# Performance work log

Hardware: AMD Instinct MI355X
Metric: run time of the kernel (lower is better)

The kernel has to match this reference:

```python
import jax, jax.numpy as jnp
import numpy as np

N = 100000
E = 1600000
E_OUT = 400000
IN_DIM = 16
HID = 64
OUT_DIM = 2
L = 6
BN_EPS = 1e-5


def setup_inputs() -> dict:
    key = jax.random.key(0)
    ks = jax.random.split(key, 12)
    x = jax.random.normal(ks[0], (N, IN_DIM), dtype=jnp.float32)
    edge_index = jax.random.randint(ks[1], (2, E), 0, N, dtype=jnp.int64)
    edge_index_out = jax.random.randint(ks[2], (2, E_OUT), 0, N, dtype=jnp.int64)
    s_emb = 1.0 / np.sqrt(IN_DIM)
    s_hid = 1.0 / np.sqrt(HID)
    W_emb = jax.random.uniform(ks[3], (IN_DIM, HID), jnp.float32, -s_emb, s_emb)
    b_emb = jax.random.uniform(ks[4], (HID,), jnp.float32, -s_emb, s_emb)
    conv_W = jax.random.uniform(ks[5], (L, HID, HID), jnp.float32, -s_hid, s_hid)
    conv_b = jnp.zeros((L, HID), jnp.float32)
    bn_gamma = jnp.ones((L, HID), jnp.float32)
    bn_beta = jnp.zeros((L, HID), jnp.float32)
    s_fc = 1.0 / np.sqrt(2 * HID)
    fc_W = jax.random.uniform(ks[6], (2 * HID, OUT_DIM), jnp.float32, -s_fc, s_fc)
    fc_b = jax.random.uniform(ks[7], (OUT_DIM,), jnp.float32, -s_fc, s_fc)
    return dict(x=x, edge_index=edge_index, edge_index_out=edge_index_out,
                W_emb=W_emb, b_emb=b_emb, conv_W=conv_W, conv_b=conv_b,
                bn_gamma=bn_gamma, bn_beta=bn_beta, fc_W=fc_W, fc_b=fc_b)


def gcn_conv(h, W, b, src, dst, norm):
    # PyG GCNConv: h' = scatter_add(norm * (hW)[src] -> dst) + b
    hw = h @ W                                   # [N, HID]
    msgs = hw[src] * norm[:, None]               # [E+N, HID] gather
    agg = jax.ops.segment_sum(msgs, dst, num_segments=N)
    return agg + b


def batchnorm_train(h, gamma, beta):
    mean = jnp.mean(h, axis=0)
    var = jnp.mean(jnp.square(h - mean), axis=0)  # biased var (BN training)
    return (h - mean) * jax.lax.rsqrt(var + BN_EPS) * gamma + beta


def reference(x, edge_index, edge_index_out, W_emb, b_emb, conv_W, conv_b,
              bn_gamma, bn_beta, fc_W, fc_b):
    # add self-loops + symmetric normalization (computed once, shared by layers)
    loop = jnp.arange(N, dtype=edge_index.dtype)
    src = jnp.concatenate([edge_index[0], loop])
    dst = jnp.concatenate([edge_index[1], loop])
    deg = jax.ops.segment_sum(jnp.ones_like(dst, dtype=jnp.float32), dst, num_segments=N)
    dinv = jnp.where(deg > 0, jax.lax.rsqrt(jnp.maximum(deg, 1.0)), 0.0)
    norm = dinv[src] * dinv[dst]

    x_embed = x @ W_emb + b_emb                  # node embedding [N, HID]
    for i in range(L):
        h = gcn_conv(x_embed, conv_W[i], conv_b[i], src, dst, norm)
        h = jax.nn.relu(batchnorm_train(h, bn_gamma[i], bn_beta[i]))
        x_embed = x_embed + h                    # residual

    e_src, e_dst = edge_index_out[0], edge_index_out[1]
    edge_repr = jnp.concatenate([x_embed[e_src], x_embed[e_dst]], axis=-1)  # [E_out, 2*HID]
    return edge_repr @ fc_W + fc_b
```

## Files before the change

kernel.cpp:

```cpp
#include <hip/hip_runtime.h>

#define NN 100000
#define NE 1600000
#define NEO 400000
#define HID 64
#define NL 6
#define BN_EPS 1e-5f

#define SPMM_BLOCKS 6250
#define GRP_ROWS 12500

#define B1CAP 210000
#define BIN_CHUNK 1024
#define BIN_J (BIN_CHUNK / 256)
#define BIN_BLOCKS ((NE + BIN_CHUNK - 1) / BIN_CHUNK)
#define SB_PER_G 32
#define SB_ROWS 391
#define SBCAP 7600
#define BIN2_CHUNK 2048
#define BIN2_BPG 103

#define OFF_ECOL 0
#define OFF_XE   NE
#define OFF_AGG  (OFF_XE + NN * 32)
#define OFF_HWB  (OFF_AGG + NN * 32)

#define OD_DINV   0
#define OD_ROWPTR 100352
#define OD_SS     300960
#define OD_SUMS   301088
#define OD_GCUR   309280
#define OD_SCNT   309312
#define OD_SBASE  309568

typedef __attribute__((ext_vector_type(8))) short bf16x8;
typedef __attribute__((ext_vector_type(4))) float f32x4;

static __device__ __forceinline__ unsigned short f2bf(float f) {
    unsigned u = __float_as_uint(f);
    unsigned r = (u + 0x7FFF + ((u >> 16) & 1)) >> 16;
    return (unsigned short)r;
}
static __device__ __forceinline__ float bflo(unsigned u) {
    return __uint_as_float(u << 16);
}
static __device__ __forceinline__ float bfhi(unsigned u) {
    return __uint_as_float(u & 0xFFFF0000u);
}

__global__ void k_bin(const int* __restrict__ src, const int* __restrict__ dst,
                      int* __restrict__ gcur, int* __restrict__ b1) {
    __shared__ int cw[4][8], bw[4][8], ow[4][8];
    int t = threadIdx.x;
    int w = t >> 6;
    if (t < 32) { ((int*)cw)[t] = 0; ((int*)ow)[t] = 0; }
    __syncthreads();
    int cb = blockIdx.x * BIN_CHUNK;
    int p[BIN_J], g[BIN_J];
#pragma unroll
    for (int j = 0; j < BIN_J; j++) {
        int e = cb + t + j * 256;
        if (e < NE) {
            int s = src[e], d = dst[e];
            g[j] = (unsigned)d / GRP_ROWS;
            p[j] = (s << 14) | (d - g[j] * GRP_ROWS);
            atomicAdd(&cw[w][g[j]], 1);
        } else {
            g[j] = -1;
        }
    }
    __syncthreads();
    if (t < 8) {
        int c0 = cw[0][t], c1 = cw[1][t], c2 = cw[2][t], c3 = cw[3][t];
        int base = t * B1CAP + atomicAdd(&gcur[t], c0 + c1 + c2 + c3);
        bw[0][t] = base;
        bw[1][t] = base + c0;
        bw[2][t] = base + c0 + c1;
        bw[3][t] = base + c0 + c1 + c2;
    }
    __syncthreads();
#pragma unroll
    for (int j = 0; j < BIN_J; j++) {
        if (g[j] >= 0) {
            int pos = bw[w][g[j]] + atomicAdd(&ow[w][g[j]], 1);
            b1[pos] = p[j];
        }
    }
}

__global__ void k_bin2(const int* __restrict__ gcur, const int* __restrict__ b1,
                       int* __restrict__ scnt, int* __restrict__ b2) {
    __shared__ int cw[4][SB_PER_G], bw[4][SB_PER_G], ow[4][SB_PER_G];
    int t = threadIdx.x;
    int w = t >> 6;
    if (t < 128) { ((int*)cw)[t] = 0; ((int*)ow)[t] = 0; }
    __syncthreads();
    int g = blockIdx.x & 7;
    int b = blockIdx.x >> 3;
    int n = gcur[g];
    const int* in = b1 + g * B1CAP;
    int c0 = b * BIN2_CHUNK;
    int p[8], sb[8];
#pragma unroll
    for (int j = 0; j < 8; j++) {
        int e = c0 + t + j * 256;
        if (e < n) {
            int v = in[e];
            int lr = v & 16383;
            sb[j] = (unsigned)lr / SB_ROWS;
            p[j] = ((v >> 14) << 9) | (lr - sb[j] * SB_ROWS);
            atomicAdd(&cw[w][sb[j]], 1);
        } else {
            sb[j] = -1;
        }
    }
    __syncthreads();
    if (t < SB_PER_G) {
        int a0 = cw[0][t], a1 = cw[1][t], a2 = cw[2][t], a3 = cw[3][t];
        int base = atomicAdd(&scnt[g * SB_PER_G + t], a0 + a1 + a2 + a3);
        bw[0][t] = base;
        bw[1][t] = base + a0;
        bw[2][t] = base + a0 + a1;
        bw[3][t] = base + a0 + a1 + a2;
    }
    __syncthreads();
#pragma unroll
    for (int j = 0; j < 8; j++) {
        if (sb[j] >= 0) {
            int pos = bw[w][sb[j]] + atomicAdd(&ow[w][sb[j]], 1);
            b2[(g * SB_PER_G + sb[j]) * SBCAP + pos] = p[j];
        }
    }
}

__global__ void k_scan256(const int* __restrict__ scnt, int* __restrict__ sbase) {
    __shared__ int sh[256];
    int t = threadIdx.x;
    int v = scnt[t];
    sh[t] = v;
    __syncthreads();
    for (int off = 1; off < 256; off <<= 1) {
        int a = (t >= off) ? sh[t - off] : 0;
        __syncthreads();
        sh[t] += a;
        __syncthreads();
    }
    sbase[t] = sh[t] - v;
}

__global__ void __launch_bounds__(256) k_build3(
        const int* __restrict__ scnt, const int* __restrict__ sbase,
        const int* __restrict__ b2, int* __restrict__ ecol,
        int* __restrict__ rowptr, float* __restrict__ dinv) {
    __shared__ int hist[SB_ROWS + 1];
    __shared__ int lofs[SB_ROWS + 1];
    __shared__ int lsrc[SBCAP];
    __shared__ int lout[SBCAP];
    int sb = blockIdx.x;
    int g = sb >> 5, sbl = sb & 31;
    int t = threadIdx.x;
    int n = scnt[sb];
    int base = sbase[sb];
    const int* in = b2 + sb * SBCAP;
    int row0 = g * GRP_ROWS + sbl * SB_ROWS;
    int nrows = GRP_ROWS - sbl * SB_ROWS;
    if (nrows > SB_ROWS) nrows = SB_ROWS;
    for (int i = t; i < nrows; i += 256) hist[i] = 0;
    __syncthreads();
    for (int i = t; i < n; i += 256) {
        int v = in[i];
        lsrc[i] = v;
        atomicAdd(&hist[v & 511], 1);
    }
    __syncthreads();
    if (t == 0) {
        int acc = 0;
        for (int r = 0; r < nrows; r++) { lofs[r] = acc; acc += hist[r]; }
        lofs[nrows] = acc;
    }
    __syncthreads();
    for (int r = t; r < nrows; r += 256) {
        rowptr[row0 + r] = base + lofs[r];
        dinv[row0 + r] = rsqrtf((float)(hist[r] + 1));
    }
    if (sb == 255 && t == 0) rowptr[NN] = base + n;
    __syncthreads();
    for (int r = t; r < nrows; r += 256) hist[r] = lofs[r];
    __syncthreads();
    for (int i = t; i < n; i += 256) {
        int v = lsrc[i];
        int pos = atomicAdd(&hist[v & 511], 1);
        lout[pos] = v >> 9;
    }
    __syncthreads();
    for (int i = t; i < n; i += 256) ecol[base + i] = lout[i];
}

__global__ void k_embed(const float* __restrict__ x, const float* __restrict__ W,
                        const float* __restrict__ b, unsigned short* __restrict__ xe16) {
    __shared__ float Ws[16 * 64];
    __shared__ float bs[64];
    int t = threadIdx.x;
    for (int i = t; i < 16 * 64; i += 256) Ws[i] = W[i];
    if (t < 64) bs[t] = b[t];
    __syncthreads();
    int c = t & 63, r = t >> 6;
    int n0 = blockIdx.x * 64;
    for (int n = n0 + r; n < n0 + 64 && n < NN; n += 4) {
        const float* xr = x + n * 16;
        float acc = bs[c];
#pragma unroll
        for (int k = 0; k < 16; k++) acc = fmaf(xr[k], Ws[k * 64 + c], acc);
        xe16[(size_t)n * 64 + c] = f2bf(acc);
    }
}

__global__ void k_hw(unsigned short* __restrict__ xe16,
                     const float* __restrict__ W, const float* __restrict__ dinv,
                     const unsigned short* __restrict__ agg16,
                     const float* __restrict__ gamma, const float* __restrict__ beta,
                     const double* __restrict__ sumsPrev, double* __restrict__ sumsCur,
                     unsigned short* __restrict__ hwb, int apply) {
    __shared__ unsigned short Wt[64 * 72];
    __shared__ unsigned short Xb[64 * 72];
    __shared__ float sss[128];
    int t = threadIdx.x;
    int n0 = blockIdx.x * 64;
    if (blockIdx.x == 0) {
        for (int i = t; i < 2048; i += 256) sumsCur[i] = 0.0;
    }
    if (apply && t < 64) {
        double s = 0.0, q = 0.0;
#pragma unroll
        for (int k = 0; k < 16; k++) {
            s += sumsPrev[k * 128 + t];
            q += sumsPrev[k * 128 + 64 + t];
        }
        double mean = s / (double)NN;
        double var = q / (double)NN - mean * mean;
        float sc = gamma[t] * rsqrtf((float)var + BN_EPS);
        sss[t] = sc;
        sss[64 + t] = beta[t] - (float)mean * sc;
    }

    {
        int c = t & 63, r = t >> 6;
#pragma unroll
        for (int jj = 0; jj < 4; jj++) {
            float w0 = W[(r * 16 + jj * 4 + 0) * 64 + c];
            float w1 = W[(r * 16 + jj * 4 + 1) * 64 + c];
            float w2 = W[(r * 16 + jj * 4 + 2) * 64 + c];
            float w3 = W[(r * 16 + jj * 4 + 3) * 64 + c];
            uint2 pk;
            pk.x = ((unsigned)f2bf(w1) << 16) | f2bf(w0);
            pk.y = ((unsigned)f2bf(w3) << 16) | f2bf(w2);
            *(uint2*)&Wt[c * 72 + r * 16 + jj * 4] = pk;
        }
    }
    __syncthreads();

    {
        int n = t >> 2, kq = t & 3;
        int node = n0 + n;
        unsigned xs[8] = {0, 0, 0, 0, 0, 0, 0, 0};
        if (node < NN) {
            const uint4* xr = (const uint4*)(xe16 + (size_t)node * 64 + kq * 16);
            uint4 x0 = xr[0], x1 = xr[1];
            xs[0] = x0.x; xs[1] = x0.y; xs[2] = x0.z; xs[3] = x0.w;
            xs[4] = x1.x; xs[5] = x1.y; xs[6] = x1.z; xs[7] = x1.w;
            if (apply) {
                const uint4* ar = (const uint4*)(agg16 + (size_t)node * 64 + kq * 16);
                uint4 a0 = ar[0], a1 = ar[1];
                unsigned as[8] = {a0.x, a0.y, a0.z, a0.w, a1.x, a1.y, a1.z, a1.w};
                int c = kq * 16;
#pragma unroll
                for (int i = 0; i < 8; i++) {
                    float v0 = bflo(xs[i]) +
                               fmaxf(fmaf(bflo(as[i]), sss[c + 2 * i], sss[64 + c + 2 * i]), 0.f);
                    float v1 = bfhi(xs[i]) +
                               fmaxf(fmaf(bfhi(as[i]), sss[c + 2 * i + 1], sss[64 + c + 2 * i + 1]), 0.f);
                    xs[i] = ((unsigned)f2bf(v1) << 16) | f2bf(v0);
                }
                uint4* xw = (uint4*)(xe16 + (size_t)node * 64 + kq * 16);
                xw[0] = make_uint4(xs[0], xs[1], xs[2], xs[3]);
                xw[1] = make_uint4(xs[4], xs[5], xs[6], xs[7]);
            }
        }
        *(uint4*)&Xb[n * 72 + kq * 16] = make_uint4(xs[0], xs[1], xs[2], xs[3]);
        *(uint4*)&Xb[n * 72 + kq * 16 + 8] = make_uint4(xs[4], xs[5], xs[6], xs[7]);
    }
    __syncthreads();

    int lane = t & 63, w = t >> 6;
    int m = lane & 15, quad = lane >> 4;
    f32x4 acc[4];
#pragma unroll
    for (int tc = 0; tc < 4; tc++) acc[tc] = (f32x4){0.f, 0.f, 0.f, 0.f};
#pragma unroll
    for (int s = 0; s < 2; s++) {
        bf16x8 bfr = *(const bf16x8*)&Xb[(w * 16 + m) * 72 + s * 32 + quad * 8];
#pragma unroll
        for (int tc = 0; tc < 4; tc++) {
            bf16x8 afr = *(const bf16x8*)&Wt[(tc * 16 + m) * 72 + s * 32 + quad * 8];
            acc[tc] = __builtin_amdgcn_mfma_f32_16x16x32_bf16(afr, bfr, acc[tc], 0, 0, 0);
        }
    }
    int node = n0 + w * 16 + m;
    if (node < NN) {
        float di = dinv[node];
#pragma unroll
        for (int tc = 0; tc < 4; tc++) {
            int c0 = tc * 16 + quad * 4;
            uint2 pk;
            pk.x = ((unsigned)f2bf(acc[tc][1] * di) << 16) | f2bf(acc[tc][0] * di);
            pk.y = ((unsigned)f2bf(acc[tc][3] * di) << 16) | f2bf(acc[tc][2] * di);
            *(uint2*)(hwb + (size_t)node * 64 + c0) = pk;
        }
    }
}

__global__ void k_spmm(const int* __restrict__ rowptr, const int* __restrict__ ecol,
                       const unsigned short* __restrict__ hwb, const float* __restrict__ dinv,
                       unsigned short* __restrict__ agg16, double* __restrict__ sums) {
    int t = threadIdx.x;
    int w = t >> 6, l = t & 63;
    int r = l >> 4;
    int sub = (l >> 3) & 1;
    int q = l & 7;
    const uint4* hw4 = (const uint4*)hwb;
    float ls[8], lq[8];
#pragma unroll
    for (int j = 0; j < 8; j++) { ls[j] = 0.f; lq[j] = 0.f; }
    for (int row0 = blockIdx.x * 16 + w * 4; row0 < NN; row0 += SPMM_BLOCKS * 16) {
        int row = row0 + r;
        bool valid = row < NN;
        int p0 = 0, p1 = 0;
        float a[8];
#pragma unroll
        for (int j = 0; j < 8; j++) a[j] = 0.f;
        if (valid) {
            p0 = rowptr[row];
            p1 = rowptr[row + 1];
            if (sub == 0) {
                uint4 sv = hw4[(size_t)row * 8 + q];
                a[0] = bflo(sv.x); a[1] = bfhi(sv.x); a[2] = bflo(sv.y); a[3] = bfhi(sv.y);
                a[4] = bflo(sv.z); a[5] = bfhi(sv.z); a[6] = bflo(sv.w); a[7] = bfhi(sv.w);
            }
        }
        int p = p0 + sub;
        for (; p + 2 < p1; p += 4) {
            int s0 = ecol[p], s1 = ecol[p + 2];
            uint4 u0 = hw4[(size_t)s0 * 8 + q];
            uint4 u1 = hw4[(size_t)s1 * 8 + q];
            a[0] += bflo(u0.x); a[1] += bfhi(u0.x); a[2] += bflo(u0.y); a[3] += bfhi(u0.y);
            a[4] += bflo(u0.z); a[5] += bfhi(u0.z); a[6] += bflo(u0.w); a[7] += bfhi(u0.w);
            a[0] += bflo(u1.x); a[1] += bfhi(u1.x); a[2] += bflo(u1.y); a[3] += bfhi(u1.y);
            a[4] += bflo(u1.z); a[5] += bfhi(u1.z); a[6] += bflo(u1.w); a[7] += bfhi(u1.w);
        }
        if (p < p1) {
            int s0 = ecol[p];
            uint4 u0 = hw4[(size_t)s0 * 8 + q];
            a[0] += bflo(u0.x); a[1] += bfhi(u0.x); a[2] += bflo(u0.y); a[3] += bfhi(u0.y);
            a[4] += bflo(u0.z); a[5] += bfhi(u0.z); a[6] += bflo(u0.w); a[7] += bfhi(u0.w);
        }
#pragma unroll
        for (int j = 0; j < 8; j++) a[j] += __shfl_xor(a[j], 8, 64);
        if (valid && sub == 0) {
            float di = dinv[row];
            unsigned pk[4];
#pragma unroll
            for (int j = 0; j < 4; j++) {
                float v0 = a[2 * j] * di, v1 = a[2 * j + 1] * di;
                pk[j] = ((unsigned)f2bf(v1) << 16) | f2bf(v0);
            }
            *(uint4*)(agg16 + (size_t)row * 64 + 8 * q) = make_uint4(pk[0], pk[1], pk[2], pk[3]);
#pragma unroll
            for (int j = 0; j < 4; j++) {
                float v0 = bflo(pk[j]), v1 = bfhi(pk[j]);
                ls[2 * j] += v0; ls[2 * j + 1] += v1;
                lq[2 * j] = fmaf(v0, v0, lq[2 * j]);
                lq[2 * j + 1] = fmaf(v1, v1, lq[2 * j + 1]);
            }
        }
    }
#pragma unroll
    for (int j = 0; j < 8; j++) {
        ls[j] += __shfl_xor(ls[j], 16, 64); ls[j] += __shfl_xor(ls[j], 32, 64);
        lq[j] += __shfl_xor(lq[j], 16, 64); lq[j] += __shfl_xor(lq[j], 32, 64);
    }
    __shared__ float Ss[4][64], Sq[4][64];
    if (l < 8) {
#pragma unroll
        for (int j = 0; j < 8; j++) {
            Ss[w][8 * l + j] = ls[j];
            Sq[w][8 * l + j] = lq[j];
        }
    }
    __syncthreads();
    if (t < 64) {
        float a = Ss[0][t] + Ss[1][t] + Ss[2][t] + Ss[3][t];
        float b = Sq[0][t] + Sq[1][t] + Sq[2][t] + Sq[3][t];
        double* sh = sums + (blockIdx.x & 15) * 128;
        atomicAdd(&sh[t], (double)a);
        atomicAdd(&sh[64 + t], (double)b);
    }
}

__global__ void k_finalize(const double* __restrict__ sums, const float* __restrict__ gamma,
                           const float* __restrict__ beta, float* __restrict__ ss) {
    int c = threadIdx.x;
    double s = 0.0, q = 0.0;
#pragma unroll
    for (int k = 0; k < 16; k++) { s += sums[k * 128 + c]; q += sums[k * 128 + 64 + c]; }
    double mean = s / (double)NN;
    double var = q / (double)NN - mean * mean;
    float sc = gamma[c] * rsqrtf((float)var + BN_EPS);
    ss[c] = sc;
    ss[64 + c] = beta[c] - (float)mean * sc;
}

__global__ void k_apply(const unsigned short* __restrict__ agg16, const float* __restrict__ ss,
                        unsigned short* __restrict__ xe16) {
    int i = blockIdx.x * blockDim.x + threadIdx.x;
    if (i < NN * 8) {
        int c0 = (i & 7) * 8;
        uint4 av = *(const uint4*)(agg16 + (size_t)i * 8);
        uint4 xv = *(const uint4*)(xe16 + (size_t)i * 8);
        unsigned as[4] = {av.x, av.y, av.z, av.w};
        unsigned xs[4] = {xv.x, xv.y, xv.z, xv.w};
#pragma unroll
        for (int j = 0; j < 4; j++) {
            int c = c0 + 2 * j;
            float v0 = bflo(xs[j]) + fmaxf(fmaf(bflo(as[j]), ss[c], ss[64 + c]), 0.f);
            float v1 = bfhi(xs[j]) + fmaxf(fmaf(bfhi(as[j]), ss[c + 1], ss[64 + c + 1]), 0.f);
            xs[j] = ((unsigned)f2bf(v1) << 16) | f2bf(v0);
        }
        *(uint4*)(xe16 + (size_t)i * 8) = make_uint4(xs[0], xs[1], xs[2], xs[3]);
    }
}

__global__ void k_out(const int* __restrict__ esrc, const int* __restrict__ edst,
                      const unsigned short* __restrict__ xe16, const float* __restrict__ fcW,
                      const float* __restrict__ fcb, float* __restrict__ out) {
    __shared__ float Ws[256];
    __shared__ float bs[2];
    int t = threadIdx.x;
    for (int i = t; i < 256; i += 256) Ws[i] = fcW[i];
    if (t < 2) bs[t] = fcb[t];
    __syncthreads();
    int e = blockIdx.x * blockDim.x + t;
    if (e < NEO) {
        int s = esrc[e], d = edst[e];
        const uint4* rs = (const uint4*)(xe16 + (size_t)s * 64);
        const uint4* rd = (const uint4*)(xe16 + (size_t)d * 64);
        float a0 = bs[0], a1 = bs[1];
#pragma unroll
        for (int i = 0; i < 8; i++) {
            uint4 v = rs[i];
            int c = i * 8;
            a0 += bflo(v.x) * Ws[(c + 0) * 2] + bfhi(v.x) * Ws[(c + 1) * 2] +
                  bflo(v.y) * Ws[(c + 2) * 2] + bfhi(v.y) * Ws[(c + 3) * 2] +
                  bflo(v.z) * Ws[(c + 4) * 2] + bfhi(v.z) * Ws[(c + 5) * 2] +
                  bflo(v.w) * Ws[(c + 6) * 2] + bfhi(v.w) * Ws[(c + 7) * 2];
            a1 += bflo(v.x) * Ws[(c + 0) * 2 + 1] + bfhi(v.x) * Ws[(c + 1) * 2 + 1] +
                  bflo(v.y) * Ws[(c + 2) * 2 + 1] + bfhi(v.y) * Ws[(c + 3) * 2 + 1] +
                  bflo(v.z) * Ws[(c + 4) * 2 + 1] + bfhi(v.z) * Ws[(c + 5) * 2 + 1] +
                  bflo(v.w) * Ws[(c + 6) * 2 + 1] + bfhi(v.w) * Ws[(c + 7) * 2 + 1];
        }
#pragma unroll
        for (int i = 0; i < 8; i++) {
            uint4 v = rd[i];
            int c = 64 + i * 8;
            a0 += bflo(v.x) * Ws[(c + 0) * 2] + bfhi(v.x) * Ws[(c + 1) * 2] +
                  bflo(v.y) * Ws[(c + 2) * 2] + bfhi(v.y) * Ws[(c + 3) * 2] +
                  bflo(v.z) * Ws[(c + 4) * 2] + bfhi(v.z) * Ws[(c + 5) * 2] +
                  bflo(v.w) * Ws[(c + 6) * 2] + bfhi(v.w) * Ws[(c + 7) * 2];
            a1 += bflo(v.x) * Ws[(c + 0) * 2 + 1] + bfhi(v.x) * Ws[(c + 1) * 2 + 1] +
                  bflo(v.y) * Ws[(c + 2) * 2 + 1] + bfhi(v.y) * Ws[(c + 3) * 2 + 1] +
                  bflo(v.z) * Ws[(c + 4) * 2 + 1] + bfhi(v.z) * Ws[(c + 5) * 2 + 1] +
                  bflo(v.w) * Ws[(c + 6) * 2 + 1] + bfhi(v.w) * Ws[(c + 7) * 2 + 1];
        }
        out[e * 2] = a0;
        out[e * 2 + 1] = a1;
    }
}

extern "C" void kernel_launch(void* const* d_in, const int* in_sizes, int n_in,
                              void* d_out, int out_size, void* d_ws, size_t ws_size,
                              hipStream_t stream) {
    const float* x      = (const float*)d_in[0];
    const int*   ei     = (const int*)d_in[1];
    const int*   eio    = (const int*)d_in[2];
    const float* W_emb  = (const float*)d_in[3];
    const float* b_emb  = (const float*)d_in[4];
    const float* conv_W = (const float*)d_in[5];
    const float* bn_g   = (const float*)d_in[7];
    const float* bn_b   = (const float*)d_in[8];
    const float* fc_W   = (const float*)d_in[9];
    const float* fc_b   = (const float*)d_in[10];
    float* out = (float*)d_out;

    float* ws   = (float*)d_ws;
    int*   ecol = (int*)(ws + OFF_ECOL);
    unsigned short* xe16  = (unsigned short*)(ws + OFF_XE);
    unsigned short* agg16 = (unsigned short*)(ws + OFF_AGG);
    unsigned short* hwb   = (unsigned short*)(ws + OFF_HWB);
    int* b1 = (int*)(ws + OFF_XE);
    int* b2 = (int*)(ws + OFF_AGG);

    float* od     = (float*)d_out;
    float* dinv   = od + OD_DINV;
    int*   rowptr = (int*)(od + OD_ROWPTR);
    float* ss     = od + OD_SS;
    double* sums  = (double*)(od + OD_SUMS);
    int*   gcur   = (int*)(od + OD_GCUR);
    int*   scnt   = (int*)(od + OD_SCNT);
    int*   sbase  = (int*)(od + OD_SBASE);

    const int* src  = ei;
    const int* dst  = ei + NE;
    const int* esrc = eio;
    const int* edst = eio + NEO;

    (void)hipMemsetAsync(gcur, 0, 8 * sizeof(int), stream);
    (void)hipMemsetAsync(scnt, 0, 256 * sizeof(int), stream);
    k_bin<<<BIN_BLOCKS, 256, 0, stream>>>(src, dst, gcur, b1);
    k_bin2<<<8 * BIN2_BPG, 256, 0, stream>>>(gcur, b1, scnt, b2);
    k_scan256<<<1, 256, 0, stream>>>(scnt, sbase);
    k_build3<<<256, 256, 0, stream>>>(scnt, sbase, b2, ecol, rowptr, dinv);

    k_embed<<<(NN + 63) / 64, 256, 0, stream>>>(x, W_emb, b_emb, xe16);

    for (int l = 0; l < NL; l++) {
        double* sumsPrev = sums + ((l + 1) & 1) * 2048;
        double* sumsCur  = sums + (l & 1) * 2048;
        k_hw<<<(NN + 63) / 64, 256, 0, stream>>>(xe16, conv_W + l * 64 * 64, dinv, agg16,
                                                 bn_g + (l ? (l - 1) * 64 : 0),
                                                 bn_b + (l ? (l - 1) * 64 : 0),
                                                 sumsPrev, sumsCur, hwb, l > 0 ? 1 : 0);
        k_spmm<<<SPMM_BLOCKS, 256, 0, stream>>>(rowptr, ecol, hwb, dinv, agg16, sumsCur);
    }
    k_finalize<<<1, 64, 0, stream>>>(sums + ((NL - 1) & 1) * 2048,
                                     bn_g + (NL - 1) * 64, bn_b + (NL - 1) * 64, ss);
    k_apply<<<(NN * 8 + 255) / 256, 256, 0, stream>>>(agg16, ss, xe16);

    k_out<<<(NEO + 255) / 256, 256, 0, stream>>>(esrc, edst, xe16, fc_W, fc_b, out);
}
```

Before: 486.1 us.

## Split SpMM into two source-node-range passes for cache locality

Each CSR row's edges are partitioned by source node, below or at/above 50000, so every row gets two segments. The SpMM then runs as two kernels: the first gathers from the lower half of hwb and writes fp32 partial sums to a scratch buffer, and the second gathers from the upper half and adds those partials. Each pass touches only half of the gathered feature table, which is meant to raise L2/MALL hit rates. In exchange it adds an extra launch per layer and an fp32 partial-sum round trip, and k_build3 now uses a parallel scan and scatters ecol directly.

Result: slower. 553.9 us (+14.0%).

```diff
diff --git a/kernel.cpp b/kernel.cpp
--- a/kernel.cpp
+++ b/kernel.cpp
@@ -9,6 +9,7 @@
 
 #define SPMM_BLOCKS 6250
 #define GRP_ROWS 12500
+#define CHUNK_NODES 50000
 
 #define B1CAP 210000
 #define BIN_CHUNK 1024
@@ -24,9 +25,10 @@
 #define OFF_XE   NE
 #define OFF_AGG  (OFF_XE + NN * 32)
 #define OFF_HWB  (OFF_AGG + NN * 32)
+#define OFF_RP4  (OFF_HWB + NN * 32)
+#define OFF_A32  (OFF_RP4 + 2 * NN + 64)
 
 #define OD_DINV   0
-#define OD_ROWPTR 100352
 #define OD_SS     300960
 #define OD_SUMS   301088
 #define OD_GCUR   309280
@@ -151,11 +153,11 @@
 __global__ void __launch_bounds__(256) k_build3(
         const int* __restrict__ scnt, const int* __restrict__ sbase,
         const int* __restrict__ b2, int* __restrict__ ecol,
-        int* __restrict__ rowptr, float* __restrict__ dinv) {
-    __shared__ int hist[SB_ROWS + 1];
-    __shared__ int lofs[SB_ROWS + 1];
+        int* __restrict__ rowptr4, float* __restrict__ dinv) {
+    __shared__ int hist[2 * SB_ROWS + 2];
+    __shared__ int lofs[2 * SB_ROWS + 2];
+    __shared__ int tmp[256];
     __shared__ int lsrc[SBCAP];
-    __shared__ int lout[SBCAP];
     int sb = blockIdx.x;
     int g = sb >> 5, sbl = sb & 31;
     int t = threadIdx.x;
@@ -165,35 +167,58 @@
     int row0 = g * GRP_ROWS + sbl * SB_ROWS;
     int nrows = GRP_ROWS - sbl * SB_ROWS;
     if (nrows > SB_ROWS) nrows = SB_ROWS;
-    for (int i = t; i < nrows; i += 256) hist[i] = 0;
+    int tot = 2 * nrows;
+    for (int i = t; i < tot; i += 256) hist[i] = 0;
     __syncthreads();
     for (int i = t; i < n; i += 256) {
         int v = in[i];
         lsrc[i] = v;
-        atomicAdd(&hist[v & 511], 1);
-    }
-    __syncthreads();
-    if (t == 0) {
-        int acc = 0;
-        for (int r = 0; r < nrows; r++) { lofs[r] = acc; acc += hist[r]; }
-        lofs[nrows] = acc;
+        int c = ((v >> 9) >= CHUNK_NODES) ? 1 : 0;
+        atomicAdd(&hist[(v & 511) * 2 + c], 1);
+    }
+    __syncthreads();
+    {
+        int b4 = t * 4;
+        int pre[4];
+        int s_ = 0;
+#pragma unroll
+        for (int j = 0; j < 4; j++) {
+            int v = (b4 + j < tot) ? hist[b4 + j] : 0;
+            pre[j] = s_;
+            s_ += v;
+        }
+        tmp[t] = s_;
+        __syncthreads();
+        for (int off = 1; off < 256; off <<= 1) {
+            int a = (t >= off) ? tmp[t - off] : 0;
+            __syncthreads();
+            tmp[t] += a;
+            __syncthreads();
+        }
+        int add = (t > 0) ? tmp[t - 1] : 0;
+#pragma unroll
+        for (int j = 0; j < 4; j++)
+            if (b4 + j <= tot) lofs[b4 + j] = add + pre[j];
+        __syncthreads();
+        if (t == 0) lofs[tot] = n;
     }
     __syncthreads();
     for (int r = t; r < nrows; r += 256) {
-        rowptr[row0 + r] = base + lofs[r];
-        dinv[row0 + r] = rsqrtf((float)(hist[r] + 1));
-    }
-    if (sb == 255 && t == 0) rowptr[NN] = base + n;
-    __syncthreads();
-    for (int r = t; r < nrows; r += 256) hist[r] = lofs[r];
+        rowptr4[(row0 + r) * 2] = base + lofs[r * 2];
+        rowptr4[(row0 + r) * 2 + 1] = base + lofs[r * 2 + 1];
+        int deg = lofs[r * 2 + 2] - lofs[r * 2];
+        dinv[row0 + r] = rsqrtf((float)(deg + 1));
+    }
+    if (sb == 255 && t == 0) rowptr4[NN * 2] = base + n;
+    __syncthreads();
+    for (int k = t; k < tot; k += 256) hist[k] = lofs[k];
     __syncthreads();
     for (int i = t; i < n; i += 256) {
         int v = lsrc[i];
-        int pos = atomicAdd(&hist[v & 511], 1);
-        lout[pos] = v >> 9;
-    }
-    __syncthreads();
-    for (int i = t; i < n; i += 256) ecol[base + i] = lout[i];
+        int c = ((v >> 9) >= CHUNK_NODES) ? 1 : 0;
+        int pos = atomicAdd(&hist[(v & 511) * 2 + c], 1);
+        ecol[base + pos] = v >> 9;
+    }
 }
 
 __global__ void k_embed(const float* __restrict__ x, const float* __restrict__ W,
@@ -319,18 +344,15 @@
     }
 }
 
-__global__ void k_spmm(const int* __restrict__ rowptr, const int* __restrict__ ecol,
-                       const unsigned short* __restrict__ hwb, const float* __restrict__ dinv,
-                       unsigned short* __restrict__ agg16, double* __restrict__ sums) {
+__global__ void k_spmmA(const int* __restrict__ rowptr4, const int* __restrict__ ecol,
+                        const unsigned short* __restrict__ hwb,
+                        float* __restrict__ agg32) {
     int t = threadIdx.x;
     int w = t >> 6, l = t & 63;
     int r = l >> 4;
     int sub = (l >> 3) & 1;
     int q = l & 7;
     const uint4* hw4 = (const uint4*)hwb;
-    float ls[8], lq[8];
-#pragma unroll
-    for (int j = 0; j < 8; j++) { ls[j] = 0.f; lq[j] = 0.f; }
     for (int row0 = blockIdx.x * 16 + w * 4; row0 < NN; row0 += SPMM_BLOCKS * 16) {
         int row = row0 + r;
         bool valid = row < NN;
@@ -339,8 +361,8 @@
 #pragma unroll
         for (int j = 0; j < 8; j++) a[j] = 0.f;
         if (valid) {
-            p0 = rowptr[row];
-            p1 = rowptr[row + 1];
+            p0 = rowptr4[row * 2];
+            p1 = rowptr4[row * 2 + 1];
             if (sub == 0) {
                 uint4 sv = hw4[(size_t)row * 8 + q];
                 a[0] = bflo(sv.x); a[1] = bfhi(sv.x); a[2] = bflo(sv.y); a[3] = bfhi(sv.y);
@@ -366,6 +388,63 @@
 #pragma unroll
         for (int j = 0; j < 8; j++) a[j] += __shfl_xor(a[j], 8, 64);
         if (valid && sub == 0) {
+            f32x4 v0 = {a[0], a[1], a[2], a[3]};
+            f32x4 v1 = {a[4], a[5], a[6], a[7]};
+            float* dst = agg32 + (size_t)row * 64 + q * 8;
+            __builtin_nontemporal_store(v0, (f32x4*)dst);
+            __builtin_nontemporal_store(v1, (f32x4*)(dst + 4));
+        }
+    }
+}
+
+__global__ void k_spmmB(const int* __restrict__ rowptr4, const int* __restrict__ ecol,
+                        const unsigned short* __restrict__ hwb, const float* __restrict__ dinv,
+                        const float* __restrict__ agg32,
+                        unsigned short* __restrict__ agg16, double* __restrict__ sums) {
+    int t = threadIdx.x;
+    int w = t >> 6, l = t & 63;
+    int r = l >> 4;
+    int sub = (l >> 3) & 1;
+    int q = l & 7;
+    const uint4* hw4 = (const uint4*)hwb;
+    float ls[8], lq[8];
+#pragma unroll
+    for (int j = 0; j < 8; j++) { ls[j] = 0.f; lq[j] = 0.f; }
+    for (int row0 = blockIdx.x * 16 + w * 4; row0 < NN; row0 += SPMM_BLOCKS * 16) {
+        int row = row0 + r;
+        bool valid = row < NN;
+        int p0 = 0, p1 = 0;
+        float a[8];
+#pragma unroll
+        for (int j = 0; j < 8; j++) a[j] = 0.f;
+        if (valid) {
+            p0 = rowptr4[row * 2 + 1];
+            p1 = rowptr4[row * 2 + 2];
+        }
+        int p = p0 + sub;
+        for (; p + 2 < p1; p += 4) {
+            int s0 = ecol[p], s1 = ecol[p + 2];
+            uint4 u0 = hw4[(size_t)s0 * 8 + q];
+            uint4 u1 = hw4[(size_t)s1 * 8 + q];
+            a[0] += bflo(u0.x); a[1] += bfhi(u0.x); a[2] += bflo(u0.y); a[3] += bfhi(u0.y);
+            a[4] += bflo(u0.z); a[5] += bfhi(u0.z); a[6] += bflo(u0.w); a[7] += bfhi(u0.w);
+            a[0] += bflo(u1.x); a[1] += bfhi(u1.x); a[2] += bflo(u1.y); a[3] += bfhi(u1.y);
+            a[4] += bflo(u1.z); a[5] += bfhi(u1.z); a[6] += bflo(u1.w); a[7] += bfhi(u1.w);
+        }
+        if (p < p1) {
+            int s0 = ecol[p];
+            uint4 u0 = hw4[(size_t)s0 * 8 + q];
+            a[0] += bflo(u0.x); a[1] += bfhi(u0.x); a[2] += bflo(u0.y); a[3] += bfhi(u0.y);
+            a[4] += bflo(u0.z); a[5] += bfhi(u0.z); a[6] += bflo(u0.w); a[7] += bfhi(u0.w);
+        }
+#pragma unroll
+        for (int j = 0; j < 8; j++) a[j] += __shfl_xor(a[j], 8, 64);
+        if (valid && sub == 0) {
+            const float* srcp = agg32 + (size_t)row * 64 + q * 8;
+            f32x4 b0 = __builtin_nontemporal_load((const f32x4*)srcp);
+            f32x4 b1 = __builtin_nontemporal_load((const f32x4*)(srcp + 4));
+            a[0] += b0[0]; a[1] += b0[1]; a[2] += b0[2]; a[3] += b0[3];
+            a[4] += b1[0]; a[5] += b1[1]; a[6] += b1[2]; a[7] += b1[3];
             float di = dinv[row];
             unsigned pk[4];
 #pragma unroll
@@ -505,12 +584,13 @@
     unsigned short* xe16  = (unsigned short*)(ws + OFF_XE);
     unsigned short* agg16 = (unsigned short*)(ws + OFF_AGG);
     unsigned short* hwb   = (unsigned short*)(ws + OFF_HWB);
+    int*   rowptr4 = (int*)(ws + OFF_RP4);
+    float* agg32   = ws + OFF_A32;
     int* b1 = (int*)(ws + OFF_XE);
     int* b2 = (int*)(ws + OFF_AGG);
 
     float* od     = (float*)d_out;
     float* dinv   = od + OD_DINV;
-    int*   rowptr = (int*)(od + OD_ROWPTR);
     float* ss     = od + OD_SS;
     double* sums  = (double*)(od + OD_SUMS);
     int*   gcur   = (int*)(od + OD_GCUR);
@@ -527,7 +607,7 @@
     k_bin<<<BIN_BLOCKS, 256, 0, stream>>>(src, dst, gcur, b1);
     k_bin2<<<8 * BIN2_BPG, 256, 0, stream>>>(gcur, b1, scnt, b2);
     k_scan256<<<1, 256, 0, stream>>>(scnt, sbase);
-    k_build3<<<256, 256, 0, stream>>>(scnt, sbase, b2, ecol, rowptr, dinv);
+    k_build3<<<256, 256, 0, stream>>>(scnt, sbase, b2, ecol, rowptr4, dinv);
 
     k_embed<<<(NN + 63) / 64, 256, 0, stream>>>(x, W_emb, b_emb, xe16);
 
@@ -538,7 +618,9 @@
                                                  bn_g + (l ? (l - 1) * 64 : 0),
                                                  bn_b + (l ? (l - 1) * 64 : 0),
                                                  sumsPrev, sumsCur, hwb, l > 0 ? 1 : 0);
-        k_spmm<<<SPMM_BLOCKS, 256, 0, stream>>>(rowptr, ecol, hwb, dinv, agg16, sumsCur);
+        k_spmmA<<<SPMM_BLOCKS, 256, 0, stream>>>(rowptr4, ecol, hwb, agg32);
+        k_spmmB<<<SPMM_BLOCKS, 256, 0, stream>>>(rowptr4, ecol, hwb, dinv, agg32,
+                                                 agg16, sumsCur);
     }
     k_finalize<<<1, 64, 0, stream>>>(sums + ((NL - 1) & 1) * 2048,
                                      bn_g + (NL - 1) * 64, bn_b + (NL - 1) * 64, ss);
```
